# Kernel tuning notes

Hardware: AMD Instinct MI355X
Metric: run time of the kernel (lower is better)

The kernel has to match this reference:

```python
import jax, jax.numpy as jnp
import numpy as np

EPS = 1e-5

def maxpool2(x):
    # 2x2 max pool, stride 2, NCHW
    B, C, H, W = x.shape
    return x.reshape(B, C, H // 2, 2, W // 2, 2).max(axis=(3, 5))

def conv1x1(x, w, b):
    # x: [B,C,H,W], w: [O,C], b: [O]
    return jnp.einsum('bchw,oc->bohw', x, w) + b[None, :, None, None]

def setup_inputs() -> dict:
    key = jax.random.key(0)
    ks = jax.random.split(key, 12)
    B, C, IC, H, W = 8, 256, 128, 128, 128
    s = 0.05
    return {
        'rgb': jax.random.normal(ks[0], (B, C, H, W), jnp.float32),
        'event': jax.random.normal(ks[1], (B, C, H, W), jnp.float32),
        'g_w': jax.random.normal(ks[2], (IC, C), jnp.float32) * s,
        'g_b': jax.random.normal(ks[3], (IC,), jnp.float32) * s,
        'theta_w': jax.random.normal(ks[4], (IC, C), jnp.float32) * s,
        'theta_b': jax.random.normal(ks[5], (IC,), jnp.float32) * s,
        'phi_w': jax.random.normal(ks[6], (IC, C), jnp.float32) * s,
        'phi_b': jax.random.normal(ks[7], (IC,), jnp.float32) * s,
        'W_w': jax.random.normal(ks[8], (C, IC), jnp.float32) * s,
        'W_b': jax.random.normal(ks[9], (C,), jnp.float32) * s,
        'bn_gamma': jax.random.normal(ks[10], (C,), jnp.float32) * s + 1.0,
        'bn_beta': jax.random.normal(ks[11], (C,), jnp.float32) * s,
    }

def reference(rgb, event, g_w, g_b, theta_w, theta_b, phi_w, phi_b, W_w, W_b, bn_gamma, bn_beta):
    B = rgb.shape[0]
    IC = g_w.shape[0]
    # initial shared 2x2 max pool on both modalities
    rgb_p = maxpool2(rgb)      # [B,C,h2,w2]
    ev_p = maxpool2(event)
    h2, w2 = rgb_p.shape[2], rgb_p.shape[3]
    # projections; g and phi have an extra sub_sample pool
    g_x = maxpool2(conv1x1(ev_p, g_w, g_b)).reshape(B, IC, -1)      # [B,IC,Nkv]
    g_x = jnp.swapaxes(g_x, 1, 2)                                    # [B,Nkv,IC]
    theta_x = conv1x1(rgb_p, theta_w, theta_b).reshape(B, IC, -1)    # [B,IC,Nq]
    theta_x = jnp.swapaxes(theta_x, 1, 2)                            # [B,Nq,IC]
    phi_x = maxpool2(conv1x1(ev_p, phi_w, phi_b)).reshape(B, IC, -1) # [B,IC,Nkv]
    # full attention: scores -> softmax -> value matmul
    f = jnp.einsum('bqc,bck->bqk', theta_x, phi_x)                   # [B,Nq,Nkv]
    f_div_C = jax.nn.softmax(f, axis=-1)
    y = jnp.einsum('bqk,bkc->bqc', f_div_C, g_x)                     # [B,Nq,IC]
    y = jnp.swapaxes(y, 1, 2).reshape(B, IC, h2, w2)
    # output 1x1 conv + BatchNorm (training-mode batch stats, biased var)
    W_y = conv1x1(y, W_w, W_b)                                       # [B,C,h2,w2]
    mean = W_y.mean(axis=(0, 2, 3), keepdims=True)
    var = W_y.var(axis=(0, 2, 3), keepdims=True)
    W_y = (W_y - mean) * jax.lax.rsqrt(var + EPS)
    W_y = W_y * bn_gamma[None, :, None, None] + bn_beta[None, :, None, None]
    z = W_y + rgb_p
    z = jnp.repeat(jnp.repeat(z, 2, axis=2), 2, axis=3)
    return z
```

## Files before the change

kernel.cpp:

```cpp
#include <hip/hip_runtime.h>
#include <stdint.h>


typedef unsigned short u16;
typedef short bf16x8 __attribute__((ext_vector_type(8)));
typedef float f32x4 __attribute__((ext_vector_type(4)));

#define MFMA16(a, b, c) __builtin_amdgcn_mfma_f32_16x16x32_bf16(a, b, c, 0, 0, 0)

__device__ __forceinline__ u16 f2bf(float x) {
    union { float f; unsigned int u; } v; v.f = x;
    unsigned int u = v.u;
    unsigned int r = u + 0x7fffu + ((u >> 16) & 1u);
    return (u16)(r >> 16);
}
__device__ __forceinline__ float bf2f(u16 h) {
    union { unsigned int u; float f; } v; v.u = ((unsigned int)h) << 16;
    return v.f;
}

__global__ void zero_kernel(float* __restrict__ p, int n) {
    int i = blockIdx.x * 256 + threadIdx.x;
    if (i < n) p[i] = 0.0f;
}

__global__ void wsplit_kernel(const float* __restrict__ tw, const float* __restrict__ pw,
                              const float* __restrict__ gw, const float* __restrict__ ww,
                              u16* __restrict__ planes) {
    int idx = blockIdx.x * 256 + threadIdx.x;
    int m = idx >> 15, e = idx & 32767;
    const float* src = (m == 0) ? tw : (m == 1) ? pw : (m == 2) ? gw : ww;
    float v = src[e];
    u16 h = f2bf(v);
    planes[m * 65536 + e] = h;
    planes[m * 65536 + 32768 + e] = f2bf(v - bf2f(h));
}

template <bool GCONV, bool POOLOUT>
__global__ __launch_bounds__(512, 4) void fused_pool_conv_kernel(
    const float* __restrict__ x,
    const u16* __restrict__ W1h, const u16* __restrict__ W1l,
    const float* __restrict__ b1,
    const u16* __restrict__ W2h, const float* __restrict__ b2,
    u16* __restrict__ o1_hi, u16* __restrict__ o1_lo, u16* __restrict__ o2,
    u16* __restrict__ pool_hi) {
    __shared__ float Pt[64 * 256];

    int bx = blockIdx.x;
    int b = bx >> 6, h2 = bx & 63;
    int tid = threadIdx.x;

    long ibase = (long)b * 256 * 16384 + (long)(2 * h2) * 128;
#pragma unroll 8
    for (int i = 0; i < 16; i++) {
        int u = i * 512 + tid;
        int c = u >> 5, w4 = u & 31;
        const float* p = &x[ibase + (long)c * 16384 + w4 * 4];
        float4 r0 = *(const float4*)p;
        float4 r1 = *(const float4*)(p + 128);
        float p0 = fmaxf(fmaxf(r0.x, r0.y), fmaxf(r1.x, r1.y));
        float p1 = fmaxf(fmaxf(r0.z, r0.w), fmaxf(r1.z, r1.w));
        int row0 = 2 * w4, row1 = 2 * w4 + 1;
        Pt[row0 * 256 + (((((c >> 2)) ^ (row0 & 31)) << 2) | (c & 3))] = p0;
        Pt[row1 * 256 + (((((c >> 2)) ^ (row1 & 31)) << 2) | (c & 3))] = p1;
    }
    __syncthreads();

    int wave = tid >> 6, lane = tid & 63, quad = lane >> 4, l16 = lane & 15;
    int mrow = (wave & 3) * 16;
    int nhalf = wave >> 2;
    int arow = mrow + l16;

    f32x4 a1[4];
    f32x4 a2[GCONV ? 4 : 1];
#pragma unroll
    for (int nt = 0; nt < 4; nt++) {
#pragma unroll
        for (int r = 0; r < 4; r++) a1[nt][r] = 0.0f;
        if (GCONV)
#pragma unroll
            for (int r = 0; r < 4; r++) a2[nt][r] = 0.0f;
    }

#pragma unroll
    for (int kc = 0; kc < 8; kc++) {
        int g0 = kc * 8 + quad * 2;
        float4 fA = *(const float4*)&Pt[arow * 256 + ((g0 ^ (arow & 31)) << 2)];
        float4 fB = *(const float4*)&Pt[arow * 256 + (((g0 + 1) ^ (arow & 31)) << 2)];
        float vv[8] = {fA.x, fA.y, fA.z, fA.w, fB.x, fB.y, fB.z, fB.w};
        bf16x8 ah, al;
#pragma unroll
        for (int e = 0; e < 8; e++) {
            u16 h = f2bf(vv[e]);
            ah[e] = (short)h;
            al[e] = (short)f2bf(vv[e] - bf2f(h));
        }
#pragma unroll
        for (int nt = 0; nt < 4; nt++) {
            long wrow = (long)(nhalf * 64 + nt * 16 + l16) * 256 + kc * 32 + quad * 8;
            bf16x8 bh = *(const bf16x8*)&W1h[wrow];
            bf16x8 bl = *(const bf16x8*)&W1l[wrow];
            a1[nt] = MFMA16(ah, bh, a1[nt]);
            a1[nt] = MFMA16(ah, bl, a1[nt]);
            a1[nt] = MFMA16(al, bh, a1[nt]);
            if (GCONV) {
                bf16x8 bg = *(const bf16x8*)&W2h[wrow];
                a2[nt] = MFMA16(ah, bg, a2[nt]);
            }
        }
    }

    long mbase = (long)b * 4096 + h2 * 64;
#pragma unroll
    for (int nt = 0; nt < 4; nt++) {
        int colo = nhalf * 64 + nt * 16 + l16;
        float bv1 = b1[colo];
        float bv2 = GCONV ? b2[colo] : 0.0f;
#pragma unroll
        for (int r = 0; r < 4; r++) {
            long row = mbase + mrow + quad * 4 + r;
            long idx = row * 128 + colo;
            float v = a1[nt][r] + bv1;
            u16 h = f2bf(v);
            o1_hi[idx] = h;
            o1_lo[idx] = f2bf(v - bf2f(h));
            if (GCONV) o2[idx] = f2bf(a2[nt][r] + bv2);
        }
    }

    if (POOLOUT) {
#pragma unroll 4
        for (int i = 0; i < 16; i++) {
            int r = i * 4 + (tid >> 7);
            int c = (tid & 127) * 2;
            int g = c >> 2;
            float2 f = *(const float2*)&Pt[r * 256 + (((g ^ (r & 31)) << 2) | (c & 3))];
            ushort2 hh;
            hh.x = f2bf(f.x);
            hh.y = f2bf(f.y);
            *(ushort2*)&pool_hi[(mbase + r) * 256 + c] = hh;
        }
    }
}

__global__ __launch_bounds__(256) void pool_phiK_kernel(
    const u16* __restrict__ fhi, const u16* __restrict__ flo,
    u16* __restrict__ khi, u16* __restrict__ klo) {
    int idx = blockIdx.x * 256 + threadIdx.x;
    int c8 = (idx & 15) * 8;
    int kv = (idx >> 4) & 1023;
    int b = idx >> 14;
    int h4 = kv >> 5, w4 = kv & 31;
    long p00 = ((long)b * 4096 + (2 * h4) * 64 + 2 * w4) * 128 + c8;
    bf16x8 h0 = *(const bf16x8*)&fhi[p00];
    bf16x8 h1 = *(const bf16x8*)&fhi[p00 + 128];
    bf16x8 h2 = *(const bf16x8*)&fhi[p00 + 8192];
    bf16x8 h3 = *(const bf16x8*)&fhi[p00 + 8320];
    bf16x8 l0 = *(const bf16x8*)&flo[p00];
    bf16x8 l1 = *(const bf16x8*)&flo[p00 + 128];
    bf16x8 l2 = *(const bf16x8*)&flo[p00 + 8192];
    bf16x8 l3 = *(const bf16x8*)&flo[p00 + 8320];
    bf16x8 oh, ol;
#pragma unroll
    for (int e = 0; e < 8; e++) {
        float v = fmaxf(fmaxf(bf2f((u16)h0[e]) + bf2f((u16)l0[e]),
                              bf2f((u16)h1[e]) + bf2f((u16)l1[e])),
                        fmaxf(bf2f((u16)h2[e]) + bf2f((u16)l2[e]),
                              bf2f((u16)h3[e]) + bf2f((u16)l3[e])));
        u16 h = f2bf(v);
        oh[e] = (short)h;
        ol[e] = (short)f2bf(v - bf2f(h));
    }
    long oi = ((long)b * 1024 + kv) * 128 + c8;
    *(bf16x8*)&khi[oi] = oh;
    *(bf16x8*)&klo[oi] = ol;
}

__global__ __launch_bounds__(256) void pool_gVt_kernel(
    const u16* __restrict__ g, u16* __restrict__ vt) {
    __shared__ u16 t[64][65];
    int bx = blockIdx.x;
    int ct = bx & 1, kvt = (bx >> 1) & 15, b = bx >> 5;
    int tid = threadIdx.x;
#pragma unroll 4
    for (int i = 0; i < 16; i++) {
        int idx = i * 256 + tid;
        int kv_l = idx >> 6, c_l = idx & 63;
        int kv = kvt * 64 + kv_l;
        int h4 = kv >> 5, w4 = kv & 31;
        long p00 = ((long)b * 4096 + (2 * h4) * 64 + 2 * w4) * 128 + ct * 64 + c_l;
        float v = fmaxf(fmaxf(bf2f(g[p00]), bf2f(g[p00 + 128])),
                        fmaxf(bf2f(g[p00 + 8192]), bf2f(g[p00 + 8192 + 128])));
        t[c_l][kv_l] = f2bf(v);
    }
    __syncthreads();
    long ob = ((long)b * 128 + ct * 64) * 1024 + kvt * 64;
#pragma unroll 4
    for (int i = 0; i < 16; i++) {
        int idx = i * 256 + tid;
        int c_l = idx >> 6, kv_l = idx & 63;
        vt[ob + (long)c_l * 1024 + kv_l] = t[c_l][kv_l];
    }
}

__global__ __launch_bounds__(512, 4) void attn_kernel(
    const u16* __restrict__ th, const u16* __restrict__ tl,
    const u16* __restrict__ khi, const u16* __restrict__ klo,
    const u16* __restrict__ vt, u16* __restrict__ y) {
    __shared__ u16 Kh[2][32][136];
    __shared__ u16 Kl[2][32][136];
    __shared__ u16 Vt[2][128][40];
    __shared__ u16 Pl[8][16][40];

    int bx = blockIdx.x;
    int b = bx & 7, qt = bx >> 3;
    int tid = threadIdx.x;
    int w = tid >> 6, g = w >> 2, wsub = w & 3;
    int lane = tid & 63, quad = lane >> 4, l16 = lane & 15;
    int qbase = qt * 64 + wsub * 16;

    bf16x8 qh[4], ql[4];
    long tb = ((long)b * 4096 + qbase + l16) * 128;
#pragma unroll
    for (int kc = 0; kc < 4; kc++) {
        qh[kc] = *(const bf16x8*)&th[tb + kc * 32 + quad * 8];
        ql[kc] = *(const bf16x8*)&tl[tb + kc * 32 + quad * 8];
    }

    f32x4 o[8];
#pragma unroll
    for (int t2 = 0; t2 < 8; t2++)
#pragma unroll
        for (int r = 0; r < 4; r++) o[t2][r] = 0.0f;
    float lp[4] = {0.0f, 0.0f, 0.0f, 0.0f};

#pragma unroll 1
    for (int it = 0; it < 16; it++) {
        __syncthreads();
#pragma unroll
        for (int j = 0; j < 2; j++) {
            int c0 = j * 512 + tid;
            int row = (c0 >> 4) & 31, ko = (c0 & 15) * 8;
            long src = ((long)b * 1024 + j * 512 + it * 32 + row) * 128 + ko;
            *(uint4*)&Kh[j][row][ko] = *(const uint4*)&khi[src];
            *(uint4*)&Kl[j][row][ko] = *(const uint4*)&klo[src];
        }
#pragma unroll
        for (int j = 0; j < 2; j++) {
            int c0 = j * 512 + tid;
            int crow = (c0 >> 2) & 127, ko = (c0 & 3) * 8;
            long src = ((long)b * 128 + crow) * 1024 + j * 512 + it * 32 + ko;
            *(uint4*)&Vt[j][crow][ko] = *(const uint4*)&vt[src];
        }
        __syncthreads();

        f32x4 s[2];
#pragma unroll
        for (int nt = 0; nt < 2; nt++)
#pragma unroll
            for (int r = 0; r < 4; r++) s[nt][r] = 0.0f;
#pragma unroll
        for (int kc = 0; kc < 4; kc++) {
#pragma unroll
            for (int nt = 0; nt < 2; nt++) {
                bf16x8 bh = *(const bf16x8*)&Kh[g][nt * 16 + l16][kc * 32 + quad * 8];
                bf16x8 bl = *(const bf16x8*)&Kl[g][nt * 16 + l16][kc * 32 + quad * 8];
                s[nt] = MFMA16(qh[kc], bh, s[nt]);
                s[nt] = MFMA16(qh[kc], bl, s[nt]);
                s[nt] = MFMA16(ql[kc], bh, s[nt]);
            }
        }

#pragma unroll
        for (int nt = 0; nt < 2; nt++)
#pragma unroll
            for (int r = 0; r < 4; r++) {
                float p = __expf(s[nt][r]);
                lp[r] += p;
                Pl[w][quad * 4 + r][nt * 16 + l16] = f2bf(p);
            }

        bf16x8 pa = *(const bf16x8*)&Pl[w][l16][quad * 8];
#pragma unroll
        for (int t2 = 0; t2 < 8; t2++) {
            bf16x8 vb = *(const bf16x8*)&Vt[g][t2 * 16 + l16][quad * 8];
            o[t2] = MFMA16(pa, vb, o[t2]);
        }
    }

#pragma unroll
    for (int r = 0; r < 4; r++)
#pragma unroll
        for (int off = 1; off < 16; off <<= 1) lp[r] += __shfl_xor(lp[r], off);

    __syncthreads();
    float* Ob = (float*)&Kh[0][0][0];
    float* Lb = (float*)&Vt[0][0][0];
    if (g == 1) {
#pragma unroll
        for (int t2 = 0; t2 < 8; t2++)
#pragma unroll
            for (int r = 0; r < 4; r++)
                Ob[(wsub * 16 + quad * 4 + r) * 132 + t2 * 16 + l16] = o[t2][r];
        if (l16 == 0)
#pragma unroll
            for (int r = 0; r < 4; r++) Lb[wsub * 16 + quad * 4 + r] = lp[r];
    }
    __syncthreads();
    if (g == 0) {
#pragma unroll
        for (int r = 0; r < 4; r++) {
            int lrow = wsub * 16 + quad * 4 + r;
            float inv = 1.0f / (lp[r] + Lb[lrow]);
            long row = (long)b * 4096 + qbase + quad * 4 + r;
#pragma unroll
            for (int t2 = 0; t2 < 8; t2++) {
                float ov = o[t2][r] + Ob[lrow * 132 + t2 * 16 + l16];
                y[row * 128 + t2 * 16 + l16] = f2bf(ov * inv);
            }
        }
    }
}

__global__ __launch_bounds__(256) void wconv_kernel(
    const u16* __restrict__ A, const u16* __restrict__ Wh,
    const float* __restrict__ bias, float* __restrict__ out_f,
    float* __restrict__ acc_g) {
    __shared__ float red[4][2][256];
    int tid = threadIdx.x;
    int wave = tid >> 6, lane = tid & 63, quad = lane >> 4, l16 = lane & 15;
    long mbase = (long)blockIdx.x * 64 + wave * 16;

    f32x4 acc[16];
#pragma unroll
    for (int nt = 0; nt < 16; nt++)
#pragma unroll
        for (int r = 0; r < 4; r++) acc[nt][r] = 0.0f;

#pragma unroll
    for (int kc = 0; kc < 4; kc++) {
        bf16x8 ah = *(const bf16x8*)&A[(mbase + l16) * 128 + kc * 32 + quad * 8];
#pragma unroll
        for (int nt = 0; nt < 16; nt++) {
            bf16x8 bh = *(const bf16x8*)&Wh[(long)(nt * 16 + l16) * 128 + kc * 32 + quad * 8];
            acc[nt] = MFMA16(ah, bh, acc[nt]);
        }
    }

#pragma unroll
    for (int nt = 0; nt < 16; nt++) {
        int colo = nt * 16 + l16;
        float bv = bias[colo];
        float vs = 0.0f, vq = 0.0f;
#pragma unroll
        for (int r = 0; r < 4; r++) {
            long row = mbase + quad * 4 + r;
            float v = acc[nt][r] + bv;
            out_f[row * 256 + colo] = v;
            vs += v;
            vq += v * v;
        }
        vs += __shfl_xor(vs, 16); vs += __shfl_xor(vs, 32);
        vq += __shfl_xor(vq, 16); vq += __shfl_xor(vq, 32);
        if (quad == 0) {
            red[wave][0][colo] = vs;
            red[wave][1][colo] = vq;
        }
    }
    __syncthreads();
    if (tid < 256) {
        int c = tid;
        float s = red[0][0][c] + red[1][0][c] + red[2][0][c] + red[3][0][c];
        float q = red[0][1][c] + red[1][1][c] + red[2][1][c] + red[3][1][c];
        atomicAdd(&acc_g[c], s);
        atomicAdd(&acc_g[256 + c], q);
    }
}

__global__ __launch_bounds__(256) void final_kernel(
    const float* __restrict__ wy, const u16* __restrict__ rgbhi,
    const float* __restrict__ acc, const float* __restrict__ gamma,
    const float* __restrict__ beta, float* __restrict__ out) {
    __shared__ float z[16][257];
    int bx = blockIdx.x;
    int wt = bx & 3, h2 = (bx >> 2) & 63, b = bx >> 8;
    int c = threadIdx.x;

    float mean = acc[c] * (1.0f / 32768.0f);
    float var = acc[256 + c] * (1.0f / 32768.0f) - mean * mean;
    float rstd = rsqrtf(var + 1e-5f);
    float gm = gamma[c] * rstd;
    float bt = beta[c] - mean * gm;

    long pbase = (long)b * 4096 + h2 * 64 + wt * 16;
#pragma unroll 4
    for (int i = 0; i < 16; i++) {
        long pi = (pbase + i) * 256 + c;
        z[i][c] = wy[pi] * gm + bt + bf2f(rgbhi[pi]);
    }
    __syncthreads();
    int tid = threadIdx.x;
#pragma unroll 4
    for (int pass = 0; pass < 64; pass++) {
        int cc = pass * 4 + (tid >> 6);
        int r = (tid >> 5) & 1, wc = tid & 31;
        float v = z[wc >> 1][cc];
        out[(((long)b * 256 + cc) * 128 + 2 * h2 + r) * 128 + wt * 32 + wc] = v;
    }
}

extern "C" void kernel_launch(void* const* d_in, const int* in_sizes, int n_in,
                              void* d_out, int out_size, void* d_ws, size_t ws_size,
                              hipStream_t stream) {
    const float* rgb     = (const float*)d_in[0];
    const float* event_  = (const float*)d_in[1];
    const float* g_w     = (const float*)d_in[2];
    const float* g_b     = (const float*)d_in[3];
    const float* theta_w = (const float*)d_in[4];
    const float* theta_b = (const float*)d_in[5];
    const float* phi_w   = (const float*)d_in[6];
    const float* phi_b   = (const float*)d_in[7];
    const float* W_w     = (const float*)d_in[8];
    const float* W_b     = (const float*)d_in[9];
    const float* gamma   = (const float*)d_in[10];
    const float* beta    = (const float*)d_in[11];

    char* ws = (char*)d_ws;
    u16* rgbpt_hi = (u16*)(ws + 0);
    u16* theta_hi = (u16*)(ws + 16777216);
    u16* theta_lo = (u16*)(ws + 25165824);
    u16* phiF_hi  = (u16*)(ws + 33554432);
    u16* phiF_lo  = (u16*)(ws + 41943040);
    u16* g_full   = (u16*)(ws + 50331648);
    u16* phiK_hi  = (u16*)(ws + 58720256);
    u16* phiK_lo  = (u16*)(ws + 60817408);
    u16* gVt      = (u16*)(ws + 62914560);
    u16* y        = (u16*)(ws + 65011712);
    float* Wy     = (float*)(ws + 73400320);
    u16* wplanes  = (u16*)(ws + 106954752);
    float* acc    = (float*)(ws + 107479040);

    zero_kernel<<<2, 256, 0, stream>>>(acc, 512);
    wsplit_kernel<<<512, 256, 0, stream>>>(theta_w, phi_w, g_w, W_w, wplanes);

    fused_pool_conv_kernel<false, true><<<512, 512, 0, stream>>>(
        rgb, wplanes + 0, wplanes + 32768, theta_b,
        nullptr, nullptr, theta_hi, theta_lo, nullptr, rgbpt_hi);
    fused_pool_conv_kernel<true, false><<<512, 512, 0, stream>>>(
        event_, wplanes + 65536, wplanes + 98304, phi_b,
        wplanes + 131072, g_b, phiF_hi, phiF_lo, g_full, nullptr);

    pool_phiK_kernel<<<512, 256, 0, stream>>>(phiF_hi, phiF_lo, phiK_hi, phiK_lo);
    pool_gVt_kernel<<<256, 256, 0, stream>>>(g_full, gVt);

    attn_kernel<<<512, 512, 0, stream>>>(theta_hi, theta_lo, phiK_hi, phiK_lo, gVt, y);

    wconv_kernel<<<512, 256, 0, stream>>>(y, wplanes + 196608, W_b, Wy, acc);

    final_kernel<<<2048, 256, 0, stream>>>(Wy, rgbpt_hi, acc, gamma, beta, (float*)d_out);
}
```

Before: 542.5 us.

## Pre-split pooled tile to bf16 hi/lo in LDS and prefetch MFMA-layout weights

The fused pool+conv kernel now converts pooled values to bf16 hi/lo planes once when writing to shared memory, instead of re-splitting fp32 values during every MFMA k-step. The weight-split kernel reorders the three projection weight planes into MFMA lane order, so each lane does one contiguous 16-byte load. Those loads are double-buffered one k-chunk ahead. Waves are retiled into 2x2 m/n tiles so each A fragment is reused across two output tiles. The launch-bounds occupancy hint is dropped, which may change register allocation and occupancy.

```diff
diff --git a/kernel.cpp b/kernel.cpp
--- a/kernel.cpp
+++ b/kernel.cpp
@@ -28,27 +28,47 @@
                               const float* __restrict__ gw, const float* __restrict__ ww,
                               u16* __restrict__ planes) {
     int idx = blockIdx.x * 256 + threadIdx.x;
-    int m = idx >> 15, e = idx & 32767;
+    int m = idx >> 15, p = idx & 32767;
     const float* src = (m == 0) ? tw : (m == 1) ? pw : (m == 2) ? gw : ww;
-    float v = src[e];
+    int se;
+    if (m < 3) {
+        int e = p & 7, lane = (p >> 3) & 63, kc = (p >> 9) & 7, ocb = p >> 12;
+        int l16 = lane & 15, quad = lane >> 4;
+        se = (ocb * 16 + l16) * 256 + kc * 32 + quad * 8 + e;
+    } else {
+        se = p;
+    }
+    float v = src[se];
     u16 h = f2bf(v);
-    planes[m * 65536 + e] = h;
-    planes[m * 65536 + 32768 + e] = f2bf(v - bf2f(h));
+    planes[m * 65536 + p] = h;
+    planes[m * 65536 + 32768 + p] = f2bf(v - bf2f(h));
 }
 
 template <bool GCONV, bool POOLOUT>
-__global__ __launch_bounds__(512, 4) void fused_pool_conv_kernel(
+__global__ __launch_bounds__(512) void fused_pool_conv_kernel(
     const float* __restrict__ x,
     const u16* __restrict__ W1h, const u16* __restrict__ W1l,
     const float* __restrict__ b1,
     const u16* __restrict__ W2h, const float* __restrict__ b2,
     u16* __restrict__ o1_hi, u16* __restrict__ o1_lo, u16* __restrict__ o2,
     u16* __restrict__ pool_hi) {
-    __shared__ float Pt[64 * 256];
+    __shared__ u16 Ph[64 * 256];
+    __shared__ u16 Plo[64 * 256];
 
     int bx = blockIdx.x;
     int b = bx >> 6, h2 = bx & 63;
     int tid = threadIdx.x;
+    int lane = tid & 63, quad = lane >> 4, l16 = lane & 15;
+    int w = tid >> 6, mhalf = w & 1, nq = w >> 1;
+
+    bf16x8 wh[2][2], wl[2][2], wg[2][2];
+#pragma unroll
+    for (int nt = 0; nt < 2; nt++) {
+        long wo = ((long)((nq * 2 + nt) * 8 + 0) * 64 + lane) * 8;
+        wh[0][nt] = *(const bf16x8*)&W1h[wo];
+        wl[0][nt] = *(const bf16x8*)&W1l[wo];
+        if (GCONV) wg[0][nt] = *(const bf16x8*)&W2h[wo];
+    }
 
     long ibase = (long)b * 256 * 16384 + (long)(2 * h2) * 128;
 #pragma unroll 8
@@ -60,84 +80,89 @@
         float4 r1 = *(const float4*)(p + 128);
         float p0 = fmaxf(fmaxf(r0.x, r0.y), fmaxf(r1.x, r1.y));
         float p1 = fmaxf(fmaxf(r0.z, r0.w), fmaxf(r1.z, r1.w));
-        int row0 = 2 * w4, row1 = 2 * w4 + 1;
-        Pt[row0 * 256 + (((((c >> 2)) ^ (row0 & 31)) << 2) | (c & 3))] = p0;
-        Pt[row1 * 256 + (((((c >> 2)) ^ (row1 & 31)) << 2) | (c & 3))] = p1;
-    }
-    __syncthreads();
-
-    int wave = tid >> 6, lane = tid & 63, quad = lane >> 4, l16 = lane & 15;
-    int mrow = (wave & 3) * 16;
-    int nhalf = wave >> 2;
-    int arow = mrow + l16;
-
-    f32x4 a1[4];
-    f32x4 a2[GCONV ? 4 : 1];
-#pragma unroll
-    for (int nt = 0; nt < 4; nt++) {
-#pragma unroll
-        for (int r = 0; r < 4; r++) a1[nt][r] = 0.0f;
-        if (GCONV)
-#pragma unroll
-            for (int r = 0; r < 4; r++) a2[nt][r] = 0.0f;
-    }
+        int row0 = 2 * w4, row1 = row0 + 1;
+        int g = c >> 3, e = c & 7;
+        u16 h0 = f2bf(p0), l0 = f2bf(p0 - bf2f(h0));
+        u16 h1 = f2bf(p1), l1 = f2bf(p1 - bf2f(h1));
+        int o0 = row0 * 256 + (((g ^ (row0 & 31)) << 3) | e);
+        int o1 = row1 * 256 + (((g ^ (row1 & 31)) << 3) | e);
+        Ph[o0] = h0; Plo[o0] = l0;
+        Ph[o1] = h1; Plo[o1] = l1;
+    }
+    __syncthreads();
+
+    f32x4 a1[2][2];
+    f32x4 a2[GCONV ? 2 : 1][2];
+#pragma unroll
+    for (int mt = 0; mt < 2; mt++)
+#pragma unroll
+        for (int nt = 0; nt < 2; nt++) {
+#pragma unroll
+            for (int r = 0; r < 4; r++) a1[mt][nt][r] = 0.0f;
+            if (GCONV)
+#pragma unroll
+                for (int r = 0; r < 4; r++) a2[mt][nt][r] = 0.0f;
+        }
 
 #pragma unroll
     for (int kc = 0; kc < 8; kc++) {
-        int g0 = kc * 8 + quad * 2;
-        float4 fA = *(const float4*)&Pt[arow * 256 + ((g0 ^ (arow & 31)) << 2)];
-        float4 fB = *(const float4*)&Pt[arow * 256 + (((g0 + 1) ^ (arow & 31)) << 2)];
-        float vv[8] = {fA.x, fA.y, fA.z, fA.w, fB.x, fB.y, fB.z, fB.w};
-        bf16x8 ah, al;
-#pragma unroll
-        for (int e = 0; e < 8; e++) {
-            u16 h = f2bf(vv[e]);
-            ah[e] = (short)h;
-            al[e] = (short)f2bf(vv[e] - bf2f(h));
-        }
-#pragma unroll
-        for (int nt = 0; nt < 4; nt++) {
-            long wrow = (long)(nhalf * 64 + nt * 16 + l16) * 256 + kc * 32 + quad * 8;
-            bf16x8 bh = *(const bf16x8*)&W1h[wrow];
-            bf16x8 bl = *(const bf16x8*)&W1l[wrow];
-            a1[nt] = MFMA16(ah, bh, a1[nt]);
-            a1[nt] = MFMA16(ah, bl, a1[nt]);
-            a1[nt] = MFMA16(al, bh, a1[nt]);
-            if (GCONV) {
-                bf16x8 bg = *(const bf16x8*)&W2h[wrow];
-                a2[nt] = MFMA16(ah, bg, a2[nt]);
-            }
-        }
+        int cur = kc & 1, nxt = cur ^ 1;
+        if (kc < 7) {
+#pragma unroll
+            for (int nt = 0; nt < 2; nt++) {
+                long wo = ((long)((nq * 2 + nt) * 8 + (kc + 1)) * 64 + lane) * 8;
+                wh[nxt][nt] = *(const bf16x8*)&W1h[wo];
+                wl[nxt][nt] = *(const bf16x8*)&W1l[wo];
+                if (GCONV) wg[nxt][nt] = *(const bf16x8*)&W2h[wo];
+            }
+        }
+        bf16x8 ah[2], al[2];
+#pragma unroll
+        for (int mt = 0; mt < 2; mt++) {
+            int arow = mhalf * 32 + mt * 16 + l16;
+            int g = kc * 4 + quad;
+            int off = arow * 256 + ((g ^ (arow & 31)) << 3);
+            ah[mt] = *(const bf16x8*)&Ph[off];
+            al[mt] = *(const bf16x8*)&Plo[off];
+        }
+#pragma unroll
+        for (int mt = 0; mt < 2; mt++)
+#pragma unroll
+            for (int nt = 0; nt < 2; nt++) {
+                a1[mt][nt] = MFMA16(ah[mt], wh[cur][nt], a1[mt][nt]);
+                a1[mt][nt] = MFMA16(ah[mt], wl[cur][nt], a1[mt][nt]);
+                a1[mt][nt] = MFMA16(al[mt], wh[cur][nt], a1[mt][nt]);
+                if (GCONV) a2[mt][nt] = MFMA16(ah[mt], wg[cur][nt], a2[mt][nt]);
+            }
     }
 
     long mbase = (long)b * 4096 + h2 * 64;
 #pragma unroll
-    for (int nt = 0; nt < 4; nt++) {
-        int colo = nhalf * 64 + nt * 16 + l16;
-        float bv1 = b1[colo];
-        float bv2 = GCONV ? b2[colo] : 0.0f;
-#pragma unroll
-        for (int r = 0; r < 4; r++) {
-            long row = mbase + mrow + quad * 4 + r;
-            long idx = row * 128 + colo;
-            float v = a1[nt][r] + bv1;
-            u16 h = f2bf(v);
-            o1_hi[idx] = h;
-            o1_lo[idx] = f2bf(v - bf2f(h));
-            if (GCONV) o2[idx] = f2bf(a2[nt][r] + bv2);
-        }
-    }
+    for (int mt = 0; mt < 2; mt++)
+#pragma unroll
+        for (int nt = 0; nt < 2; nt++) {
+            int colo = nq * 32 + nt * 16 + l16;
+            float bv1 = b1[colo];
+            float bv2 = GCONV ? b2[colo] : 0.0f;
+#pragma unroll
+            for (int r = 0; r < 4; r++) {
+                long row = mbase + mhalf * 32 + mt * 16 + quad * 4 + r;
+                long idx = row * 128 + colo;
+                float v = a1[mt][nt][r] + bv1;
+                u16 h = f2bf(v);
+                o1_hi[idx] = h;
+                o1_lo[idx] = f2bf(v - bf2f(h));
+                if (GCONV) o2[idx] = f2bf(a2[mt][nt][r] + bv2);
+            }
+        }
 
     if (POOLOUT) {
 #pragma unroll 4
         for (int i = 0; i < 16; i++) {
             int r = i * 4 + (tid >> 7);
             int c = (tid & 127) * 2;
-            int g = c >> 2;
-            float2 f = *(const float2*)&Pt[r * 256 + (((g ^ (r & 31)) << 2) | (c & 3))];
-            ushort2 hh;
-            hh.x = f2bf(f.x);
-            hh.y = f2bf(f.y);
+            int g = c >> 3;
+            ushort2 hh = *(const ushort2*)&Ph[r * 256 + (((g ^ (r & 31)) << 3) | (c & 7))];
             *(ushort2*)&pool_hi[(mbase + r) * 256 + c] = hh;
         }
     }
```

New measurement: 486.1 us. 10.4% less time.
